# Kernel optimization log

Hardware: AMD Instinct MI355X
Metric: run time of the kernel (lower is better)

The kernel has to match this reference:

```python
import jax, jax.numpy as jnp
import numpy as np

N_NODES = 100000


def gcn_conv(x, W, b, src, dst, n_nodes):
    # PyG GCNConv: x' = x @ W; symmetric deg^-1/2 normalization with self-loops; scatter-add; + bias
    h = x @ W  # [N, out]
    ones = jnp.ones(dst.shape[0], dtype=h.dtype)
    deg = jax.ops.segment_sum(ones, dst, num_segments=n_nodes)  # in-degree incl. self-loops
    dinv = jnp.where(deg > 0, jax.lax.rsqrt(deg), 0.0)
    norm = dinv[src] * dinv[dst]                      # [E]
    msgs = h[src] * norm[:, None]                     # gather + scale, [E, out]
    out = jax.ops.segment_sum(msgs, dst, num_segments=n_nodes)  # scatter-add
    return out + b


def setup_inputs() -> dict:
    key = jax.random.key(0)
    ks = jax.random.split(key, 8)
    n, e, din, dh, dout = N_NODES, 1600000, 32, 64, 5
    x = jax.random.normal(ks[0], (n, din), dtype=jnp.float32)
    edge_index = jax.random.randint(ks[1], (2, e), 0, n, dtype=jnp.int64)
    W1 = jax.random.normal(ks[2], (din, dh), dtype=jnp.float32) * (1.0 / np.sqrt(din))
    b1 = jax.random.normal(ks[3], (dh,), dtype=jnp.float32) * 0.02
    W2 = jax.random.normal(ks[4], (dh, dh), dtype=jnp.float32) * (1.0 / np.sqrt(dh))
    b2 = jax.random.normal(ks[5], (dh,), dtype=jnp.float32) * 0.02
    Wfc = jax.random.normal(ks[6], (dh, dout), dtype=jnp.float32) * (1.0 / np.sqrt(dh))
    bfc = jax.random.normal(ks[7], (dout,), dtype=jnp.float32) * 0.02
    return {"x": x, "edge_index": edge_index, "W1": W1, "b1": b1,
            "W2": W2, "b2": b2, "Wfc": Wfc, "bfc": bfc}


def reference(x, edge_index, W1, b1, W2, b2, Wfc, bfc):
    n = x.shape[0]
    loops = jnp.arange(n, dtype=edge_index.dtype)
    src = jnp.concatenate([edge_index[0], loops])  # add self-loops (PyG default)
    dst = jnp.concatenate([edge_index[1], loops])
    h = jax.nn.relu(gcn_conv(x, W1, b1, src, dst, n))
    h = jax.nn.relu(gcn_conv(h, W2, b2, src, dst, n))
    g = jnp.mean(h, axis=0)          # mean pool over nodes, [hidden]
    logits = g @ Wfc + bfc           # [output_dim]
    return jax.nn.log_softmax(logits, axis=0)
```

## Files before the change

### kernel.cpp

```cpp
#include <hip/hip_runtime.h>
#include <math.h>

#define NBLK 256

typedef unsigned int uint;
typedef __attribute__((ext_vector_type(8))) short short8;
typedef __attribute__((ext_vector_type(4))) float f32x4;
typedef __attribute__((ext_vector_type(2))) float f32x2;

#if defined(__has_builtin)
#if __has_builtin(__builtin_amdgcn_cvt_pk_f32_fp8) && __has_builtin(__builtin_amdgcn_cvt_pk_fp8_f32)
#define HW_FP8 1
#endif
#endif
#ifndef HW_FP8
#define HW_FP8 0
#endif

__device__ __forceinline__ uint pack_bf16(float a, float b) {
    uint ua = __float_as_uint(a), ub = __float_as_uint(b);
    ua = (ua + 0x7fffu + ((ua >> 16) & 1u)) >> 16;
    ub = (ub + 0x7fffu + ((ub >> 16) & 1u)) >> 16;
    return ua | (ub << 16);
}

__device__ __forceinline__ uint fp8_enc_sw(float v) {
    uint u = __float_as_uint(v);
    uint s = (u >> 24) & 0x80u;
    uint a = u & 0x7fffffffu;
    if (a < 0x3BF80000u) return s;
    if (a >= 0x43F80000u) return s | 0x7Fu;
    uint r = a + 0x0007FFFFu + ((a >> 20) & 1u);
    uint e8 = (r >> 23) - 120u;
    return s | (e8 << 3) | ((r >> 20) & 7u);
}
__device__ __forceinline__ float fp8_dec_sw(uint b) {
    uint t = b & 0x7fu;
    uint h = ((b & 0x80u) << 8) | (t ? ((t << 7) + 0x2000u) : 0u);
    return (float)__builtin_bit_cast(_Float16, (unsigned short)h);
}

__device__ __forceinline__ uint fp8x2_enc(float a, float b) {
#if HW_FP8
    return (uint)__builtin_amdgcn_cvt_pk_fp8_f32(a, b, 0, false);
#else
    return fp8_enc_sw(a) | (fp8_enc_sw(b) << 8);
#endif
}

#if HW_FP8
#define DEC8ACC(U)                                                         \
    do {                                                                   \
        f32x2 p0 = __builtin_amdgcn_cvt_pk_f32_fp8((int)(U).x, 0);         \
        f32x2 p1 = __builtin_amdgcn_cvt_pk_f32_fp8((int)(U).x, 1);         \
        f32x2 p2 = __builtin_amdgcn_cvt_pk_f32_fp8((int)(U).y, 0);         \
        f32x2 p3 = __builtin_amdgcn_cvt_pk_f32_fp8((int)(U).y, 1);         \
        a0 += p0.x; a1 += p0.y; a2 += p1.x; a3 += p1.y;                    \
        a4 += p2.x; a5 += p2.y; a6 += p3.x; a7 += p3.y;                    \
    } while (0)
#else
#define DEC8ACC(U)                                                         \
    do {                                                                   \
        a0 += fp8_dec_sw((U).x); a1 += fp8_dec_sw((U).x >> 8);             \
        a2 += fp8_dec_sw((U).x >> 16); a3 += fp8_dec_sw((U).x >> 24);      \
        a4 += fp8_dec_sw((U).y); a5 += fp8_dec_sw((U).y >> 8);             \
        a6 += fp8_dec_sw((U).y >> 16); a7 += fp8_dec_sw((U).y >> 24);      \
    } while (0)
#endif


__global__ void pass_hist(const int* __restrict__ dst, int* __restrict__ cnt,
                          int E, int nbucket, int chunk) {
    extern __shared__ int h[];
    int blk = blockIdx.x;
    for (int i = threadIdx.x; i < nbucket; i += blockDim.x) h[i] = 0;
    __syncthreads();
    int lo = blk * chunk, hi = min(lo + chunk, E);
    for (int e = lo + threadIdx.x; e < hi; e += blockDim.x)
        atomicAdd(&h[dst[e] >> 8], 1);
    __syncthreads();
    for (int i = threadIdx.x; i < nbucket; i += blockDim.x)
        cnt[i * NBLK + blk] = h[i];
}

__global__ void row_scan(int* __restrict__ cnt, int* __restrict__ totals) {
    __shared__ int lds[NBLK];
    int b = blockIdx.x, t = threadIdx.x;
    int v = cnt[b * NBLK + t];
    lds[t] = v;
    __syncthreads();
    for (int off = 1; off < NBLK; off <<= 1) {
        int y = (t >= off) ? lds[t - off] : 0;
        __syncthreads();
        lds[t] += y;
        __syncthreads();
    }
    cnt[b * NBLK + t] = lds[t] - v;
    if (t == NBLK - 1) totals[b] = lds[NBLK - 1];
}

__global__ void total_scan(int* __restrict__ totals, int nb, float* __restrict__ part2) {
    __shared__ int lds[256];
    __shared__ int carry;
    int t = threadIdx.x;
    for (int i = t; i < 64 * 64; i += 256) part2[i] = 0.f;
    if (t == 0) carry = 0;
    __syncthreads();
    for (int c = 0; c < nb; c += 256) {
        int v = (c + t < nb) ? totals[c + t] : 0;
        lds[t] = v;
        __syncthreads();
        for (int off = 1; off < 256; off <<= 1) {
            int y = (t >= off) ? lds[t - off] : 0;
            __syncthreads();
            lds[t] += y;
            __syncthreads();
        }
        if (c + t < nb) totals[c + t] = carry + lds[t] - v;
        __syncthreads();
        if (t == 0) carry += lds[255];
        __syncthreads();
    }
    if (t == 0) totals[nb] = carry;
}

__global__ void pass_scatter(const int* __restrict__ src, const int* __restrict__ dst,
                             const int* __restrict__ cnt, const int* __restrict__ totals,
                             int* __restrict__ bucketed, int E, int nbucket, int chunk) {
    extern __shared__ int lcur[];
    int blk = blockIdx.x;
    for (int i = threadIdx.x; i < nbucket; i += blockDim.x)
        lcur[i] = cnt[i * NBLK + blk] + totals[i];
    __syncthreads();
    int lo = blk * chunk, hi = min(lo + chunk, E);
    for (int e = lo + threadIdx.x; e < hi; e += blockDim.x) {
        int s = src[e], d = dst[e];
        int pos = atomicAdd(&lcur[d >> 8], 1);
        bucketed[pos] = (s << 8) | (d & 255);
    }
}

__global__ void bucket_finalize(const int* __restrict__ bucketed, const int* __restrict__ totals,
                                int* __restrict__ rowptr, float* __restrict__ dinv,
                                int* __restrict__ csr_src, const float* __restrict__ x,
                                uint* __restrict__ xfp8, int n) {
    __shared__ int deg[256], sc[256], lcur[256];
    int b = blockIdx.x, t = threadIdx.x;
    int base = totals[b], bend = totals[b + 1];
    deg[t] = 0;
    __syncthreads();
    for (int i = base + t; i < bend; i += 256)
        atomicAdd(&deg[bucketed[i] & 255], 1);
    __syncthreads();
    int v = deg[t];
    sc[t] = v;
    __syncthreads();
    for (int off = 1; off < 256; off <<= 1) {
        int y = (t >= off) ? sc[t - off] : 0;
        __syncthreads();
        sc[t] += y;
        __syncthreads();
    }
    int ex = sc[t] - v;
    lcur[t] = ex;
    int node = b * 256 + t;
    if (node < n) {
        float dfac = rsqrtf((float)(v + 1));
        rowptr[node] = base + ex;
        dinv[node] = dfac;
        const float4* xr = reinterpret_cast<const float4*>(x + (size_t)node * 32);
        uint* xo = xfp8 + (size_t)node * 8;
#pragma unroll
        for (int w = 0; w < 8; ++w) {
            float4 xv = xr[w];
            uint lo = fp8x2_enc(xv.x * dfac, xv.y * dfac);
            uint hi = fp8x2_enc(xv.z * dfac, xv.w * dfac);
            xo[w] = (lo & 0xffffu) | (hi << 16);
        }
    }
    if (b == 0 && t == 0) rowptr[n] = totals[gridDim.x];
    __syncthreads();
    for (int i = base + t; i < bend; i += 256) {
        int p = bucketed[i];
        int pos = atomicAdd(&lcur[p & 255], 1);
        csr_src[base + pos] = p >> 8;
    }
}


__device__ __forceinline__ short8 make_bfrag(const float* __restrict__ W, int kbase, int col) {
    uint w0 = pack_bf16(W[(kbase + 0) * 64 + col], W[(kbase + 1) * 64 + col]);
    uint w1 = pack_bf16(W[(kbase + 2) * 64 + col], W[(kbase + 3) * 64 + col]);
    uint w2 = pack_bf16(W[(kbase + 4) * 64 + col], W[(kbase + 5) * 64 + col]);
    uint w3 = pack_bf16(W[(kbase + 6) * 64 + col], W[(kbase + 7) * 64 + col]);
    uint4 u; u.x = w0; u.y = w1; u.z = w2; u.w = w3;
    return __builtin_bit_cast(short8, u);
}

__global__ __launch_bounds__(256, 4) void agg1_gemm1_fused(
    const int* __restrict__ rowptr, const int* __restrict__ csr_src,
    const float* __restrict__ dinv, const uint* __restrict__ xfp8,
    const float* __restrict__ W, const float* __restrict__ bias,
    uint* __restrict__ outw, int n, int npad) {
    __shared__ uint lds[64 * 16];
    int t = threadIdx.x;
    {
        int v4 = t >> 2, q = t & 3;
        int node = blockIdx.x * 64 + v4;
        const uint* fs = xfp8 + q * 2;
        float a0 = 0.f, a1 = 0.f, a2 = 0.f, a3 = 0.f,
              a4 = 0.f, a5 = 0.f, a6 = 0.f, a7 = 0.f;
        float di = 0.f;
        int k = 0, end = 0;
        if (node < n) {
            k = rowptr[node]; end = rowptr[node + 1];
            di = dinv[node];
            uint2 w = *reinterpret_cast<const uint2*>(fs + (size_t)node * 8);
            DEC8ACC(w);
        }
        for (; k + 4 <= end; k += 4) {
            int s0 = csr_src[k], s1 = csr_src[k + 1], s2 = csr_src[k + 2], s3 = csr_src[k + 3];
            uint2 u0 = *reinterpret_cast<const uint2*>(fs + (size_t)s0 * 8);
            uint2 u1 = *reinterpret_cast<const uint2*>(fs + (size_t)s1 * 8);
            uint2 u2 = *reinterpret_cast<const uint2*>(fs + (size_t)s2 * 8);
            uint2 u3 = *reinterpret_cast<const uint2*>(fs + (size_t)s3 * 8);
            DEC8ACC(u0); DEC8ACC(u1); DEC8ACC(u2); DEC8ACC(u3);
        }
        for (; k < end; ++k) {
            int s = csr_src[k];
            uint2 u = *reinterpret_cast<const uint2*>(fs + (size_t)s * 8);
            DEC8ACC(u);
        }
        uint4 o;
        o.x = pack_bf16(a0 * di, a1 * di);
        o.y = pack_bf16(a2 * di, a3 * di);
        o.z = pack_bf16(a4 * di, a5 * di);
        o.w = pack_bf16(a6 * di, a7 * di);
        *reinterpret_cast<uint4*>(&lds[v4 * 16 + q * 4]) = o;
    }
    __syncthreads();
    int lane = t & 63, wv = t >> 6;
    int rowbase = blockIdx.x * 64 + wv * 16;
    int r16 = lane & 15, g4 = lane >> 4;
    short8 a = __builtin_bit_cast(short8,
        *reinterpret_cast<const uint4*>(&lds[(wv * 16 + r16) * 16 + g4 * 4]));
    int kbase = g4 * 8;
    float dr[4];
#pragma unroll
    for (int r = 0; r < 4; ++r) {
        int row = rowbase + g4 * 4 + r;
        dr[r] = (row < n) ? dinv[row] : 0.f;
    }
#pragma unroll
    for (int nt = 0; nt < 4; ++nt) {
        int col = nt * 16 + r16;
        short8 b = make_bfrag(W, kbase, col);
        f32x4 z = {0.f, 0.f, 0.f, 0.f};
        f32x4 acc = __builtin_amdgcn_mfma_f32_16x16x32_bf16(a, b, z, 0, 0, 0);
        float bcol = bias[col];
#pragma unroll
        for (int r = 0; r < 4; ++r) {
            int row = rowbase + g4 * 4 + r;
            float v = fmaxf(acc[r] + bcol, 0.f) * dr[r];
            float vn = __shfl_xor(v, 1);
            uint e = fp8x2_enc(v, vn) & 0xffffu;
            uint e2 = __shfl_xor(e, 2);
            if ((r16 & 3) == 0)
                outw[(size_t)row * 16 + (col >> 2)] = e | (e2 << 16);
        }
    }
}

__global__ __launch_bounds__(512, 2) void agg2_gather64(
    const int* __restrict__ rowptr, const int* __restrict__ csr_src,
    const float* __restrict__ dinv, const uint* __restrict__ feat,
    uint* __restrict__ out, int n, int npad) {
    int node = blockIdx.x * 64 + (threadIdx.x >> 3);
    if (node >= n) return;
    int q = threadIdx.x & 7;
    const uint* fs = feat + q * 2;
    int k = rowptr[node], end = rowptr[node + 1];
    float a0 = 0.f, a1 = 0.f, a2 = 0.f, a3 = 0.f, a4 = 0.f, a5 = 0.f, a6 = 0.f, a7 = 0.f;
    {
        uint2 w = *reinterpret_cast<const uint2*>(fs + (size_t)node * 16);
        DEC8ACC(w);
    }
    for (; k + 4 <= end; k += 4) {
        int s0 = csr_src[k], s1 = csr_src[k + 1], s2 = csr_src[k + 2], s3 = csr_src[k + 3];
        uint2 u0 = *reinterpret_cast<const uint2*>(fs + (size_t)s0 * 16);
        uint2 u1 = *reinterpret_cast<const uint2*>(fs + (size_t)s1 * 16);
        uint2 u2 = *reinterpret_cast<const uint2*>(fs + (size_t)s2 * 16);
        uint2 u3 = *reinterpret_cast<const uint2*>(fs + (size_t)s3 * 16);
        DEC8ACC(u0); DEC8ACC(u1); DEC8ACC(u2); DEC8ACC(u3);
    }
    for (; k < end; ++k) {
        int s = csr_src[k];
        uint2 u = *reinterpret_cast<const uint2*>(fs + (size_t)s * 16);
        DEC8ACC(u);
    }
    float di = dinv[node];
    uint4 o;
    o.x = pack_bf16(a0 * di, a1 * di);
    o.y = pack_bf16(a2 * di, a3 * di);
    o.z = pack_bf16(a4 * di, a5 * di);
    o.w = pack_bf16(a6 * di, a7 * di);
    *reinterpret_cast<uint4*>(
        out + ((size_t)(q >> 1) * npad + node) * 8 + (q & 1) * 4) = o;
}

__global__ __launch_bounds__(256) void gemm2_mfma_pool(const uint* __restrict__ A,
                                                       const float* __restrict__ W,
                                                       const float* __restrict__ bias,
                                                       float* __restrict__ part2,
                                                       int n, int npad) {
    __shared__ float sblk[64];
    int t = threadIdx.x;
    if (t < 64) sblk[t] = 0.f;
    __syncthreads();
    int lane = t & 63, wv = t >> 6;
    int rowbase = blockIdx.x * 64 + wv * 16;
    int r16 = lane & 15, g4 = lane >> 4;
    size_t roff = (size_t)(rowbase + r16) * 8 + (g4 & 1) * 4;
    size_t sstride = (size_t)npad * 8;
    short8 a0 = __builtin_bit_cast(short8,
        *reinterpret_cast<const uint4*>(A + (size_t)(g4 >> 1) * sstride + roff));
    short8 a1 = __builtin_bit_cast(short8,
        *reinterpret_cast<const uint4*>(A + (size_t)(2 + (g4 >> 1)) * sstride + roff));
#pragma unroll
    for (int nt = 0; nt < 4; ++nt) {
        int col = nt * 16 + r16;
        short8 b0 = make_bfrag(W, g4 * 8, col);
        short8 b1 = make_bfrag(W, 32 + g4 * 8, col);
        f32x4 z = {0.f, 0.f, 0.f, 0.f};
        f32x4 acc = __builtin_amdgcn_mfma_f32_16x16x32_bf16(a0, b0, z, 0, 0, 0);
        acc = __builtin_amdgcn_mfma_f32_16x16x32_bf16(a1, b1, acc, 0, 0, 0);
        float bcol = bias[col];
        float part = 0.f;
#pragma unroll
        for (int r = 0; r < 4; ++r) {
            int row = rowbase + g4 * 4 + r;
            float v = fmaxf(acc[r] + bcol, 0.f);
            part += (row < n) ? v : 0.f;
        }
        atomicAdd(&sblk[col], part);
    }
    __syncthreads();
    if (t < 64) atomicAdd(&part2[(size_t)(blockIdx.x & 63) * 64 + t], sblk[t]);
}

__global__ __launch_bounds__(512) void final_head(const float* __restrict__ part2,
                                                  const float* __restrict__ Wfc,
                                                  const float* __restrict__ bfc,
                                                  float* __restrict__ out, int n) {
    __shared__ float red[512];
    __shared__ float gsh[64];
    __shared__ float logits[5];
    int t = threadIdx.x;
    int col = t & 63, grp = t >> 6;
    float acc = 0.f;
#pragma unroll
    for (int i = 0; i < 8; ++i) acc += part2[(size_t)(grp * 8 + i) * 64 + col];
    red[t] = acc;
    __syncthreads();
    if (t < 64) {
        float s = 0.f;
#pragma unroll
        for (int gI = 0; gI < 8; ++gI) s += red[gI * 64 + t];
        gsh[t] = s;
    }
    __syncthreads();
    if (t < 5) {
        float a = bfc[t];
        float invn = 1.0f / (float)n;
        for (int k = 0; k < 64; ++k) a += (gsh[k] * invn) * Wfc[k * 5 + t];
        logits[t] = a;
    }
    __syncthreads();
    if (t == 0) {
        float m = logits[0];
        for (int i = 1; i < 5; ++i) m = fmaxf(m, logits[i]);
        float s = 0.0f;
        for (int i = 0; i < 5; ++i) s += expf(logits[i] - m);
        float lse = m + logf(s);
        for (int i = 0; i < 5; ++i) out[i] = logits[i] - lse;
    }
}


extern "C" void kernel_launch(void* const* d_in, const int* in_sizes, int n_in,
                              void* d_out, int out_size, void* d_ws, size_t ws_size,
                              hipStream_t stream) {
    const float* x   = (const float*)d_in[0];
    const int*   ei  = (const int*)d_in[1];
    const float* W1  = (const float*)d_in[2];
    const float* b1  = (const float*)d_in[3];
    const float* W2  = (const float*)d_in[4];
    const float* b2  = (const float*)d_in[5];
    const float* Wfc = (const float*)d_in[6];
    const float* bfc = (const float*)d_in[7];
    float* out = (float*)d_out;

    const int n = in_sizes[0] / 32;
    const int E = in_sizes[1] / 2;
    const int* src = ei;
    const int* dst = ei + E;
    const int npad = (n + 63) & ~63;
    const int nbucket = (n + 255) >> 8;
    const int chunk = (E + NBLK - 1) / NBLK;
    const int nchunk = (n + 63) / 64;

    int*   csr_src = (int*)d_ws;
    int*   rowptr  = csr_src + E;
    float* dinv    = (float*)(rowptr + n + 1);
    int*   cnt     = (int*)(dinv + n);
    int*   totals  = cnt + (size_t)nbucket * NBLK;
    size_t offw    = (size_t)(totals + nbucket + 1 - (int*)d_ws);
    offw           = (offw + 15) & ~(size_t)15;
    uint*  xfp8    = (uint*)d_ws + offw;
    uint*  h1fp8   = xfp8 + (size_t)npad * 8;
    uint*  agg2    = h1fp8 + (size_t)npad * 16;
    float* part2   = (float*)(agg2 + (size_t)4 * npad * 8);
    int*   bucketed = (int*)agg2;

    const int B = 256;
    const size_t lds_b = (size_t)nbucket * sizeof(int);

    pass_hist<<<NBLK, B, lds_b, stream>>>(dst, cnt, E, nbucket, chunk);
    row_scan<<<nbucket, NBLK, 0, stream>>>(cnt, totals);
    total_scan<<<1, B, 0, stream>>>(totals, nbucket, part2);
    pass_scatter<<<NBLK, B, lds_b, stream>>>(src, dst, cnt, totals, bucketed, E, nbucket, chunk);
    bucket_finalize<<<nbucket, B, 0, stream>>>(bucketed, totals, rowptr, dinv, csr_src,
                                               x, xfp8, n);

    agg1_gemm1_fused<<<nchunk, B, 0, stream>>>(rowptr, csr_src, dinv, xfp8, W1, b1,
                                               h1fp8, n, npad);

    agg2_gather64<<<nchunk, 512, 0, stream>>>(rowptr, csr_src, dinv, h1fp8, agg2, n, npad);
    gemm2_mfma_pool<<<nchunk, B, 0, stream>>>(agg2, W2, b2, part2, n, npad);

    final_head<<<1, 512, 0, stream>>>(part2, Wfc, bfc, out, n);
}
```

Before: 112.6 us.

## Fuse layer-2 aggregation with GEMM2 and pooling through swizzled LDS

Merges the layer-2 neighbor gather and the MFMA GEMM/ReLU/pool kernel into one launch. The aggregated bf16 rows are staged in an XOR-swizzled shared-memory tile instead of a global intermediate buffer, and the 8 waves split the 64 output columns in pairs of 16-column tiles. This removes one kernel launch and the global write and re-read of the agg2 buffer, at the cost of more LDS per block and a barrier between the gather and the matrix multiply.

```diff
diff --git a/kernel.cpp b/kernel.cpp
--- a/kernel.cpp
+++ b/kernel.cpp
@@ -271,69 +271,69 @@
     }
 }
 
-__global__ __launch_bounds__(512, 2) void agg2_gather64(
+__global__ __launch_bounds__(512, 2) void agg2_gemm2_fused(
     const int* __restrict__ rowptr, const int* __restrict__ csr_src,
     const float* __restrict__ dinv, const uint* __restrict__ feat,
-    uint* __restrict__ out, int n, int npad) {
-    int node = blockIdx.x * 64 + (threadIdx.x >> 3);
-    if (node >= n) return;
-    int q = threadIdx.x & 7;
-    const uint* fs = feat + q * 2;
-    int k = rowptr[node], end = rowptr[node + 1];
-    float a0 = 0.f, a1 = 0.f, a2 = 0.f, a3 = 0.f, a4 = 0.f, a5 = 0.f, a6 = 0.f, a7 = 0.f;
-    {
-        uint2 w = *reinterpret_cast<const uint2*>(fs + (size_t)node * 16);
-        DEC8ACC(w);
-    }
-    for (; k + 4 <= end; k += 4) {
-        int s0 = csr_src[k], s1 = csr_src[k + 1], s2 = csr_src[k + 2], s3 = csr_src[k + 3];
-        uint2 u0 = *reinterpret_cast<const uint2*>(fs + (size_t)s0 * 16);
-        uint2 u1 = *reinterpret_cast<const uint2*>(fs + (size_t)s1 * 16);
-        uint2 u2 = *reinterpret_cast<const uint2*>(fs + (size_t)s2 * 16);
-        uint2 u3 = *reinterpret_cast<const uint2*>(fs + (size_t)s3 * 16);
-        DEC8ACC(u0); DEC8ACC(u1); DEC8ACC(u2); DEC8ACC(u3);
-    }
-    for (; k < end; ++k) {
-        int s = csr_src[k];
-        uint2 u = *reinterpret_cast<const uint2*>(fs + (size_t)s * 16);
-        DEC8ACC(u);
-    }
-    float di = dinv[node];
-    uint4 o;
-    o.x = pack_bf16(a0 * di, a1 * di);
-    o.y = pack_bf16(a2 * di, a3 * di);
-    o.z = pack_bf16(a4 * di, a5 * di);
-    o.w = pack_bf16(a6 * di, a7 * di);
-    *reinterpret_cast<uint4*>(
-        out + ((size_t)(q >> 1) * npad + node) * 8 + (q & 1) * 4) = o;
-}
-
-__global__ __launch_bounds__(256) void gemm2_mfma_pool(const uint* __restrict__ A,
-                                                       const float* __restrict__ W,
-                                                       const float* __restrict__ bias,
-                                                       float* __restrict__ part2,
-                                                       int n, int npad) {
+    const float* __restrict__ W, const float* __restrict__ bias,
+    float* __restrict__ part2, int n, int npad) {
+    __shared__ uint lds[64 * 32];
     __shared__ float sblk[64];
     int t = threadIdx.x;
     if (t < 64) sblk[t] = 0.f;
+    {
+        int v8 = t >> 3, q = t & 7;
+        int node = blockIdx.x * 64 + v8;
+        const uint* fs = feat + q * 2;
+        float a0 = 0.f, a1 = 0.f, a2 = 0.f, a3 = 0.f,
+              a4 = 0.f, a5 = 0.f, a6 = 0.f, a7 = 0.f;
+        float di = 0.f;
+        int k = 0, end = 0;
+        if (node < n) {
+            k = rowptr[node]; end = rowptr[node + 1];
+            di = dinv[node];
+            uint2 w = *reinterpret_cast<const uint2*>(fs + (size_t)node * 16);
+            DEC8ACC(w);
+        }
+        for (; k + 4 <= end; k += 4) {
+            int s0 = csr_src[k], s1 = csr_src[k + 1], s2 = csr_src[k + 2], s3 = csr_src[k + 3];
+            uint2 u0 = *reinterpret_cast<const uint2*>(fs + (size_t)s0 * 16);
+            uint2 u1 = *reinterpret_cast<const uint2*>(fs + (size_t)s1 * 16);
+            uint2 u2 = *reinterpret_cast<const uint2*>(fs + (size_t)s2 * 16);
+            uint2 u3 = *reinterpret_cast<const uint2*>(fs + (size_t)s3 * 16);
+            DEC8ACC(u0); DEC8ACC(u1); DEC8ACC(u2); DEC8ACC(u3);
+        }
+        for (; k < end; ++k) {
+            int s = csr_src[k];
+            uint2 u = *reinterpret_cast<const uint2*>(fs + (size_t)s * 16);
+            DEC8ACC(u);
+        }
+        uint4 o;
+        o.x = pack_bf16(a0 * di, a1 * di);
+        o.y = pack_bf16(a2 * di, a3 * di);
+        o.z = pack_bf16(a4 * di, a5 * di);
+        o.w = pack_bf16(a6 * di, a7 * di);
+        int ga = q ^ (v8 & 7);
+        *reinterpret_cast<uint4*>(&lds[v8 * 32 + ga * 4]) = o;
+    }
     __syncthreads();
     int lane = t & 63, wv = t >> 6;
-    int rowbase = blockIdx.x * 64 + wv * 16;
+    int rg = wv & 3;
+    int rowbase = blockIdx.x * 64 + rg * 16;
     int r16 = lane & 15, g4 = lane >> 4;
-    size_t roff = (size_t)(rowbase + r16) * 8 + (g4 & 1) * 4;
-    size_t sstride = (size_t)npad * 8;
-    short8 a0 = __builtin_bit_cast(short8,
-        *reinterpret_cast<const uint4*>(A + (size_t)(g4 >> 1) * sstride + roff));
-    short8 a1 = __builtin_bit_cast(short8,
-        *reinterpret_cast<const uint4*>(A + (size_t)(2 + (g4 >> 1)) * sstride + roff));
-#pragma unroll
-    for (int nt = 0; nt < 4; ++nt) {
-        int col = nt * 16 + r16;
+    int arow = rg * 16 + r16;
+    short8 a0f = __builtin_bit_cast(short8, *reinterpret_cast<const uint4*>(
+        &lds[arow * 32 + (g4 ^ (r16 & 7)) * 4]));
+    short8 a1f = __builtin_bit_cast(short8, *reinterpret_cast<const uint4*>(
+        &lds[arow * 32 + ((4 + g4) ^ (r16 & 7)) * 4]));
+    int nt0 = (wv >> 2) * 2;
+#pragma unroll
+    for (int i = 0; i < 2; ++i) {
+        int col = (nt0 + i) * 16 + r16;
         short8 b0 = make_bfrag(W, g4 * 8, col);
         short8 b1 = make_bfrag(W, 32 + g4 * 8, col);
         f32x4 z = {0.f, 0.f, 0.f, 0.f};
-        f32x4 acc = __builtin_amdgcn_mfma_f32_16x16x32_bf16(a0, b0, z, 0, 0, 0);
-        acc = __builtin_amdgcn_mfma_f32_16x16x32_bf16(a1, b1, acc, 0, 0, 0);
+        f32x4 acc = __builtin_amdgcn_mfma_f32_16x16x32_bf16(a0f, b0, z, 0, 0, 0);
+        acc = __builtin_amdgcn_mfma_f32_16x16x32_bf16(a1f, b1, acc, 0, 0, 0);
         float bcol = bias[col];
         float part = 0.f;
 #pragma unroll
@@ -418,9 +418,8 @@
     offw           = (offw + 15) & ~(size_t)15;
     uint*  xfp8    = (uint*)d_ws + offw;
     uint*  h1fp8   = xfp8 + (size_t)npad * 8;
-    uint*  agg2    = h1fp8 + (size_t)npad * 16;
-    float* part2   = (float*)(agg2 + (size_t)4 * npad * 8);
-    int*   bucketed = (int*)agg2;
+    int*   bucketed = (int*)(h1fp8 + (size_t)npad * 16);
+    float* part2   = (float*)(bucketed + E);
 
     const int B = 256;
     const size_t lds_b = (size_t)nbucket * sizeof(int);
@@ -435,8 +434,8 @@
     agg1_gemm1_fused<<<nchunk, B, 0, stream>>>(rowptr, csr_src, dinv, xfp8, W1, b1,
                                                h1fp8, n, npad);
 
-    agg2_gather64<<<nchunk, 512, 0, stream>>>(rowptr, csr_src, dinv, h1fp8, agg2, n, npad);
-    gemm2_mfma_pool<<<nchunk, B, 0, stream>>>(agg2, W2, b2, part2, n, npad);
+    agg2_gemm2_fused<<<nchunk, 512, 0, stream>>>(rowptr, csr_src, dinv, h1fp8, W2, b2,
+                                                 part2, n, npad);
 
     final_head<<<1, 512, 0, stream>>>(part2, Wfc, bfc, out, n);
 }
```

After: 105.1 us. -6.7%, faster.
